# Performance work log

Measured on AMD Instinct MI355X. Metric: run time of the kernel, lower is better.

Reference implementation:

```python
import jax, jax.numpy as jnp
import numpy as np

N, E, D, H, C = 40000, 640000, 128, 4, 32  # nodes, edges, in_hid, heads, out_channels/head
NUM_NODE_TYPE, NUM_EDGE_TYPE = 8, 8
NEG_SLOPE = 0.2
EDGE_TYPE_SELF = 0


def setup_inputs() -> dict:
    key = jax.random.key(0)
    ks = jax.random.split(key, 12)
    x = jax.random.normal(ks[0], (N, D), dtype=jnp.float32)
    # build edges with no self-loops (the module filters src==dst before adding self-loops)
    src = jax.random.randint(ks[1], (E,), 0, N, dtype=jnp.int32)
    off = jax.random.randint(ks[2], (E,), 1, N, dtype=jnp.int32)
    dst = (src + off) % N
    edge_index = jnp.stack([src, dst])  # [2, E]
    node_type = jax.random.randint(ks[3], (N,), 0, NUM_NODE_TYPE, dtype=jnp.int32)
    edge_type = jax.random.randint(ks[4], (E,), 0, NUM_EDGE_TYPE, dtype=jnp.int32)
    g = 0.05
    Wq = jax.random.normal(ks[5], (H * C, D), dtype=jnp.float32) * g
    Wk = jax.random.normal(ks[6], (H * C, D), dtype=jnp.float32) * g
    Wv = jax.random.normal(ks[7], (H * C, D), dtype=jnp.float32) * g
    att_i = jax.random.normal(ks[8], (1, H, C), dtype=jnp.float32) * g
    att_j = jax.random.normal(ks[9], (1, H, C), dtype=jnp.float32) * g
    bias = jnp.zeros((H * C,), dtype=jnp.float32)
    node_emb_table = jax.random.normal(ks[10], (NUM_NODE_TYPE, D), dtype=jnp.float32) * g
    edge_emb_table = jax.random.normal(ks[11], (NUM_EDGE_TYPE, D), dtype=jnp.float32) * g
    return {"x": x, "edge_index": edge_index, "node_type": node_type,
            "edge_type": edge_type, "Wq": Wq, "Wk": Wk, "Wv": Wv,
            "att_i": att_i, "att_j": att_j, "bias": bias,
            "node_emb_table": node_emb_table, "edge_emb_table": edge_emb_table}


def reference(x, edge_index, node_type, edge_type, Wq, Wk, Wv,
              att_i, att_j, bias, node_emb_table, edge_emb_table):
    n = x.shape[0]
    # node-type embedding add
    x = x + node_emb_table[node_type]                       # [N, D]
    xq = x @ Wq.T                                           # [N, H*C]
    # add self-loops (input edges contain no src==dst by construction)
    self_idx = jnp.arange(n, dtype=edge_index.dtype)
    src = jnp.concatenate([edge_index[0], self_idx])        # [E+N]
    dst = jnp.concatenate([edge_index[1], self_idx])        # [E+N]
    et = jnp.concatenate([edge_type,
                          jnp.full((n,), EDGE_TYPE_SELF, dtype=edge_type.dtype)])
    edge_emb = edge_emb_table[et]                           # [E+N, D]
    # message: per-edge gather + K/V linear + additive attention
    x_j = x[src] + edge_emb                                 # [E+N, D]
    xq_i = xq[dst].reshape(-1, H, C)                        # [E+N, H, C]
    x_k = (x_j @ Wk.T).reshape(-1, H, C)
    x_v = (x_j @ Wv.T).reshape(-1, H, C)
    alpha = (xq_i * att_i).sum(-1) + (x_k * att_j).sum(-1)  # [E+N, H]
    alpha = jax.nn.leaky_relu(alpha, NEG_SLOPE)
    # segment softmax over destination nodes (PyG softmax, eps=1e-16)
    amax = jax.ops.segment_max(alpha, dst, num_segments=n)  # [N, H]
    alpha = jnp.exp(alpha - amax[dst])
    denom = jax.ops.segment_sum(alpha, dst, num_segments=n)
    alpha = alpha / (denom[dst] + 1e-16)
    # scatter-add weighted values
    out = jax.ops.segment_sum(x_v * alpha[..., None], dst, num_segments=n)  # [N, H, C]
    return out.reshape(n, H * C) + bias
```

## Files before the change

### kernel.cpp

```cpp
#include <hip/hip_runtime.h>
#include <math.h>

#define NN 40000
#define NE 640000
#define D 128
#define NH 4
#define NC 32
#define NEG 0.2f

#define NBKT 1250
#define NBIN 250
#define SEGC 16

typedef __attribute__((ext_vector_type(8))) short bf16x8;
typedef __attribute__((ext_vector_type(4))) float f32x4;

__device__ __forceinline__ unsigned pack_bf16(float a, float b) {
  unsigned ua = __float_as_uint(a), ub = __float_as_uint(b);
  ua = (ua + 0x7FFFu + ((ua >> 16) & 1u)) >> 16;
  ub = (ub + 0x7FFFu + ((ub >> 16) & 1u)) & 0xFFFF0000u;
  return ub | ua;
}

__device__ __forceinline__ bf16x8 to_bf16x8(float4 a, float4 b) {
  union { bf16x8 v; unsigned u[4]; } r;
  r.u[0] = pack_bf16(a.x, a.y);
  r.u[1] = pack_bf16(a.z, a.w);
  r.u[2] = pack_bf16(b.x, b.y);
  r.u[3] = pack_bf16(b.z, b.w);
  return r.v;
}

__device__ __forceinline__ float4 f4add(float4 a, float4 b) {
  return make_float4(a.x + b.x, a.y + b.y, a.z + b.z, a.w + b.w);
}

__global__ __launch_bounds__(1024) void k_pb(
    const int* __restrict__ ei, const int* __restrict__ etype,
    unsigned* __restrict__ binbuf,
    const float* __restrict__ Wq, const float* __restrict__ Wk,
    const float* __restrict__ Wv,
    const float* __restrict__ att_i, const float* __restrict__ att_j,
    const float* __restrict__ eemb,
    float* __restrict__ ev, float* __restrict__ a_et,
    unsigned* __restrict__ Wvh) {
  __shared__ unsigned smem[10640];
  int b = blockIdx.x, t = threadIdx.x;

  if (b < NBIN) {
    unsigned* lbuf = smem;
    int* hist = (int*)(smem + 10000);
    int e0 = b * 2560;
#pragma unroll 1
    for (int pass = 0; pass < 2; ++pass) {
      int bk0 = pass * 625;
      for (int j = t; j < 625; j += 1024) hist[j] = 0;
      __syncthreads();
#pragma unroll
      for (int k = 0; k < 3; ++k) {
        int ee = k * 1024 + t;
        if (ee < 2560) {
          int e = e0 + ee;
          int src = ei[e];
          int dst = ei[NE + e];
          int et  = etype[e];
          int bk = (dst >> 5) - bk0;
          if (bk >= 0 && bk < 625) {
            int r = atomicAdd(&hist[bk], 1);
            if (r < SEGC)
              lbuf[bk * SEGC + r] =
                  (unsigned)src | ((unsigned)et << 16) | ((unsigned)(dst & 31) << 19);
          }
        }
      }
      __syncthreads();
      for (int j = t; j < 625; j += 1024) {
        unsigned c = (unsigned)min(hist[j], SEGC);
        unsigned s0 = (c == 0) ? 0u : (lbuf[j * SEGC] & 0x01FFFFFFu);
        lbuf[j * SEGC] = s0 | (c << 27);
      }
      __syncthreads();
      for (int j = t; j < 625; j += 1024) {
        const uint4* __restrict__ s4 = (const uint4*)(lbuf + j * SEGC);
        uint4* __restrict__ d4 =
            (uint4*)(binbuf + ((size_t)(bk0 + j) * NBIN + b) * SEGC);
        d4[0] = s4[0]; d4[1] = s4[1]; d4[2] = s4[2]; d4[3] = s4[3];
      }
      __syncthreads();
    }
    return;
  }

  float* sm = (float*)smem;
  int tb = b - NBIN;
  if (tb == 0) {
    for (int j = t; j < 1024; j += 1024) {
      int isq = (j < 512);
      int h = (j >> 7) & 3, d = j & 127;
      const float* __restrict__ Wm = isq ? Wq : Wk;
      const float* __restrict__ am = isq ? att_i : att_j;
      float s = 0.f;
#pragma unroll
      for (int c = 0; c < NC; ++c) s = fmaf(am[h * NC + c], Wm[(h * NC + c) * D + d], s);
      sm[j] = s;
    }
    __syncthreads();
    for (int j = t; j < 1024; j += 1024) {
      int r = j >> 6;
      int c2 = (j & 63) * 2;
      float a = 0.f, bb = 0.f;
      if (r < 8) { a = sm[r * 128 + c2]; bb = sm[r * 128 + c2 + 1]; }
      Wvh[(128 + r) * 64 + (j & 63)] = pack_bf16(a, bb);
    }
    if (t < 32) {
      int ty = t >> 2, hh = t & 3;
      const float* wrow = sm + 512 + hh * 128;
      const float* __restrict__ emb = eemb + ty * D;
      float s = 0.f;
#pragma unroll 8
      for (int d = 0; d < D; ++d) s = fmaf(wrow[d], emb[d], s);
      a_et[t] = s;
    }
  } else if (tb <= 8) {
    int ty = tb - 1;
    if (t < 128) sm[t] = eemb[ty * D + t];
    __syncthreads();
    if (t < 128) {
      const float4* __restrict__ wr = (const float4*)(Wv + (size_t)t * D);
      const float4* __restrict__ er = (const float4*)sm;
      float s = 0.f;
#pragma unroll
      for (int k = 0; k < 32; ++k) {
        float4 ww = wr[k], ee = er[k];
        s = fmaf(ww.x, ee.x, s); s = fmaf(ww.y, ee.y, s);
        s = fmaf(ww.z, ee.z, s); s = fmaf(ww.w, ee.w, s);
      }
      ev[ty * D + t] = s;
    }
  } else {
    int j0 = (tb - 9) * 1024;
    for (int j = j0 + t; j < j0 + 1024; j += 1024)
      Wvh[j] = pack_bf16(Wv[2 * j], Wv[2 * j + 1]);
  }
}

__global__ __launch_bounds__(64) void k_xv(
    const float* __restrict__ x, const int* __restrict__ node_type,
    const float* __restrict__ nemb, const unsigned* __restrict__ Wvh,
    unsigned* __restrict__ xvh, float* __restrict__ aq, float* __restrict__ ak) {
  int bb = blockIdx.x, l = threadIdx.x;
  int quad = l >> 4, col = l & 15;
  int n0w = bb * 16;
  int node = n0w + col;
  int ntA = node_type[node];
  const float4* __restrict__ xr = (const float4*)(x + (size_t)node * D);
  const float4* __restrict__ nr = (const float4*)(nemb + (size_t)ntA * D);
  bf16x8 afr[4];
#pragma unroll
  for (int s = 0; s < 4; ++s) {
    const float4* p = xr + s * 8 + quad * 2;
    const float4* q4 = nr + s * 8 + quad * 2;
    afr[s] = to_bf16x8(f4add(p[0], q4[0]), f4add(p[1], q4[1]));
  }
  f32x4 acc[9];
#pragma unroll
  for (int ct = 0; ct < 9; ++ct) acc[ct] = (f32x4){0.f, 0.f, 0.f, 0.f};
#pragma unroll
  for (int ct = 0; ct < 9; ++ct) {
    const unsigned* __restrict__ brow = Wvh + (size_t)(ct * 16 + col) * 64;
#pragma unroll
    for (int s = 0; s < 4; ++s) {
      bf16x8 bfr = *(const bf16x8*)(brow + s * 16 + quad * 4);
      acc[ct] = __builtin_amdgcn_mfma_f32_16x16x32_bf16(afr[s], bfr, acc[ct], 0, 0, 0);
    }
  }
  int nodes[4];
#pragma unroll
  for (int r = 0; r < 4; ++r) nodes[r] = n0w + quad * 4 + r;
#pragma unroll
  for (int ct = 0; ct < 8; ++ct) {
#pragma unroll
    for (int r = 0; r < 4; ++r) {
      float val = acc[ct][r];
      float pv = __shfl_xor(val, 1);
      if (!(col & 1)) {
        xvh[nodes[r] * 64 + ct * 8 + (col >> 1)] = pack_bf16(val, pv);
      }
    }
  }
  if (col < 4) {
#pragma unroll
    for (int r = 0; r < 4; ++r) aq[nodes[r] * NH + col] = acc[8][r];
  } else if (col < 8) {
#pragma unroll
    for (int r = 0; r < 4; ++r) ak[nodes[r] * NH + (col - 4)] = acc[8][r];
  }
}

__global__ __launch_bounds__(512) void k_gb(
    const unsigned* __restrict__ binbuf,
    const float* __restrict__ aq, const float* __restrict__ ak,
    const float* __restrict__ a_et, const unsigned* __restrict__ xvh,
    const float* __restrict__ ev, const float* __restrict__ bias,
    float* __restrict__ out) {
  __shared__ int lcnt[32];
  __shared__ unsigned csr[2048];
  int b = blockIdx.x, t = threadIdx.x;
  if (t < 32) lcnt[t] = 0;
  __syncthreads();
  if (t < 2 * NBIN) {
    int seg = t >> 1, half = t & 1;
    const unsigned* __restrict__ sp = binbuf + ((size_t)b * NBIN + seg) * SEGC;
    int cnt = (int)(sp[0] >> 27);
    int base = half * 8;
    if (cnt > base) {
      uint4 a0 = *(const uint4*)(sp + base);
      uint4 a1 = *(const uint4*)(sp + base + 4);
      unsigned rr[8] = {a0.x, a0.y, a0.z, a0.w, a1.x, a1.y, a1.z, a1.w};
      if (half == 0) rr[0] &= 0x01FFFFFFu;
      int jn = min(cnt - base, 8);
#pragma unroll
      for (int j = 0; j < 8; ++j) {
        if (j < jn) {
          unsigned rec = rr[j];
          int loc = (int)(rec >> 19) & 31;
          int r = atomicAdd(&lcnt[loc], 1);
          if (r < 63) csr[(loc << 6) + r] = rec & 0x7FFFFu;
        }
      }
    }
  }
  __syncthreads();
  int w = t >> 6, l = t & 63;
  int g = l >> 3, q = l & 7;
  int h = q >> 1;
  const uint4* __restrict__ xv4 = (const uint4*)xvh;
  const float4* __restrict__ ep = (const float4*)(ev + g * D + 16 * q);
  float4 ea0 = ep[0], ea1 = ep[1], ea2 = ep[2], ea3 = ep[3];
#pragma unroll 1
  for (int j4 = 0; j4 < 4; ++j4) {
    int loc = (w << 2) + j4;
    int n = (b << 5) + loc;
    float aqh = aq[n * NH + h];
    int deg = min(lcnt[loc], 63);
    int m = deg + 1;
    float acc[16];
#pragma unroll
    for (int k = 0; k < 16; ++k) acc[k] = 0.f;
    float ps[8];
#pragma unroll
    for (int k = 0; k < 8; ++k) ps[k] = 0.f;
    int iters = (m + 7) >> 3;
    int i = g;
    bool val = (i < m);
    unsigned rec = (val && i < deg) ? csr[(loc << 6) + i] : (unsigned)n;
    int src = (int)(rec & 0xFFFFu), etc = (int)(rec >> 16);
    float sA = ak[src * NH + h] + a_et[etc * NH + h];
    uint4 vb0 = xv4[src * 16 + 2 * q];
    uint4 vb1 = xv4[src * 16 + 2 * q + 1];
    for (int it = 0; it < iters; ++it) {
      int i2 = i + 8;
      bool v2 = (i2 < m);
      float sAn = 0.f; int etn = 0;
      uint4 vb0n = make_uint4(0, 0, 0, 0), vb1n = make_uint4(0, 0, 0, 0);
      if (it + 1 < iters) {
        unsigned rec2 = (v2 && i2 < deg) ? csr[(loc << 6) + i2] : (unsigned)n;
        int s2 = (int)(rec2 & 0xFFFFu);
        etn = (int)(rec2 >> 16);
        sAn = ak[s2 * NH + h] + a_et[etn * NH + h];
        vb0n = xv4[s2 * 16 + 2 * q];
        vb1n = xv4[s2 * 16 + 2 * q + 1];
      }
      float s = aqh + sA;
      s = (s > 0.f) ? s : NEG * s;
      float p = val ? __expf(s) : 0.f;
#pragma unroll
      for (int tt = 0; tt < 8; ++tt) ps[tt] += (etc == tt) ? p : 0.f;
      float f[16];
      f[0]  = __uint_as_float(vb0.x << 16); f[1]  = __uint_as_float(vb0.x & 0xFFFF0000u);
      f[2]  = __uint_as_float(vb0.y << 16); f[3]  = __uint_as_float(vb0.y & 0xFFFF0000u);
      f[4]  = __uint_as_float(vb0.z << 16); f[5]  = __uint_as_float(vb0.z & 0xFFFF0000u);
      f[6]  = __uint_as_float(vb0.w << 16); f[7]  = __uint_as_float(vb0.w & 0xFFFF0000u);
      f[8]  = __uint_as_float(vb1.x << 16); f[9]  = __uint_as_float(vb1.x & 0xFFFF0000u);
      f[10] = __uint_as_float(vb1.y << 16); f[11] = __uint_as_float(vb1.y & 0xFFFF0000u);
      f[12] = __uint_as_float(vb1.z << 16); f[13] = __uint_as_float(vb1.z & 0xFFFF0000u);
      f[14] = __uint_as_float(vb1.w << 16); f[15] = __uint_as_float(vb1.w & 0xFFFF0000u);
#pragma unroll
      for (int k = 0; k < 16; ++k) acc[k] = fmaf(p, f[k], acc[k]);
      i = i2; val = v2; sA = sAn; etc = etn; vb0 = vb0n; vb1 = vb1n;
    }
#pragma unroll
    for (int tt = 0; tt < 8; ++tt) {
      ps[tt] += __shfl_xor(ps[tt], 8);
      ps[tt] += __shfl_xor(ps[tt], 16);
      ps[tt] += __shfl_xor(ps[tt], 32);
    }
    float dsum = ((ps[0] + ps[1]) + (ps[2] + ps[3])) + ((ps[4] + ps[5]) + (ps[6] + ps[7]));
    float psg = ps[0];
#pragma unroll
    for (int tt = 1; tt < 8; ++tt) psg = (g == tt) ? ps[tt] : psg;
    acc[0]  = fmaf(psg, ea0.x, acc[0]);
    acc[1]  = fmaf(psg, ea0.y, acc[1]);
    acc[2]  = fmaf(psg, ea0.z, acc[2]);
    acc[3]  = fmaf(psg, ea0.w, acc[3]);
    acc[4]  = fmaf(psg, ea1.x, acc[4]);
    acc[5]  = fmaf(psg, ea1.y, acc[5]);
    acc[6]  = fmaf(psg, ea1.z, acc[6]);
    acc[7]  = fmaf(psg, ea1.w, acc[7]);
    acc[8]  = fmaf(psg, ea2.x, acc[8]);
    acc[9]  = fmaf(psg, ea2.y, acc[9]);
    acc[10] = fmaf(psg, ea2.z, acc[10]);
    acc[11] = fmaf(psg, ea2.w, acc[11]);
    acc[12] = fmaf(psg, ea3.x, acc[12]);
    acc[13] = fmaf(psg, ea3.y, acc[13]);
    acc[14] = fmaf(psg, ea3.z, acc[14]);
    acc[15] = fmaf(psg, ea3.w, acc[15]);
#pragma unroll
    for (int k = 0; k < 16; ++k) {
      acc[k] += __shfl_xor(acc[k], 8);
      acc[k] += __shfl_xor(acc[k], 16);
      acc[k] += __shfl_xor(acc[k], 32);
    }
    if (g == 0) {
      float inv = 1.f / (dsum + 1e-16f);
      const float4* __restrict__ b4 = (const float4*)(bias + 16 * q);
      float4* __restrict__ op = (float4*)(out + (size_t)n * D + 16 * q);
#pragma unroll
      for (int k4 = 0; k4 < 4; ++k4) {
        float4 bb = b4[k4];
        op[k4] = make_float4(acc[4 * k4 + 0] * inv + bb.x,
                             acc[4 * k4 + 1] * inv + bb.y,
                             acc[4 * k4 + 2] * inv + bb.z,
                             acc[4 * k4 + 3] * inv + bb.w);
      }
    }
  }
}

extern "C" void kernel_launch(void* const* d_in, const int* in_sizes, int n_in,
                              void* d_out, int out_size, void* d_ws, size_t ws_size,
                              hipStream_t stream) {
  const float* x      = (const float*)d_in[0];
  const int*   ei     = (const int*)d_in[1];
  const int*   ntype  = (const int*)d_in[2];
  const int*   etype  = (const int*)d_in[3];
  const float* Wq     = (const float*)d_in[4];
  const float* Wk     = (const float*)d_in[5];
  const float* Wv     = (const float*)d_in[6];
  const float* att_i  = (const float*)d_in[7];
  const float* att_j  = (const float*)d_in[8];
  const float* bias   = (const float*)d_in[9];
  const float* nemb   = (const float*)d_in[10];
  const float* eemb   = (const float*)d_in[11];
  float* out = (float*)d_out;

  float* ws     = (float*)d_ws;
  unsigned* xvh = (unsigned*)ws;
  float* aq     = ws + (size_t)NN * 64;
  float* ak     = aq + NN * NH;
  float* ev     = ak + NN * NH;
  float* a_et   = ev + 1024;
  unsigned* Wvh = (unsigned*)(a_et + 32);
  unsigned* binbuf = (unsigned*)(Wvh + 9216);

  k_pb<<<dim3(NBIN + 17), dim3(1024), 0, stream>>>(ei, etype, binbuf,
                                                   Wq, Wk, Wv, att_i, att_j, eemb,
                                                   ev, a_et, Wvh);
  k_xv<<<dim3(2500), dim3(64), 0, stream>>>(x, ntype, nemb, Wvh, xvh, aq, ak);
  k_gb<<<dim3(NBKT), dim3(512), 0, stream>>>(binbuf, aq, ak, a_et,
                                             xvh, ev, bias, out);
}
```

Baseline: 166.3 us.

## Replace fixed-capacity edge bins with compact per-block counting-sort and offset table

The edge binning kernel now runs a two-pass counting sort per block: a histogram of destination buckets, a shared-memory prefix scan, then a compact scatter of packed edge records into a contiguous per-block buffer, plus a global offset/count table. The gather kernel reads each block's offset and count and walks the records serially instead of reading fixed 16-slot segments. This removes the padded 16-entry-per-segment writes and reads, shrinking global traffic and dropping the silent capacity overflow. In exchange it adds a Hillis-Steele scan with many barriers and a serial variable-length loop per thread in the gather stage.

```diff
diff --git a/kernel.cpp b/kernel.cpp
--- a/kernel.cpp
+++ b/kernel.cpp
@@ -10,7 +10,6 @@
 
 #define NBKT 1250
 #define NBIN 250
-#define SEGC 16
 
 typedef __attribute__((ext_vector_type(8))) short bf16x8;
 typedef __attribute__((ext_vector_type(4))) float f32x4;
@@ -37,57 +36,67 @@
 
 __global__ __launch_bounds__(1024) void k_pb(
     const int* __restrict__ ei, const int* __restrict__ etype,
-    unsigned* __restrict__ binbuf,
+    unsigned* __restrict__ obuf, unsigned* __restrict__ binbuf,
     const float* __restrict__ Wq, const float* __restrict__ Wk,
     const float* __restrict__ Wv,
     const float* __restrict__ att_i, const float* __restrict__ att_j,
     const float* __restrict__ eemb,
     float* __restrict__ ev, float* __restrict__ a_et,
     unsigned* __restrict__ Wvh) {
-  __shared__ unsigned smem[10640];
+  __shared__ unsigned smem[6400];
   int b = blockIdx.x, t = threadIdx.x;
 
   if (b < NBIN) {
-    unsigned* lbuf = smem;
-    int* hist = (int*)(smem + 10000);
+    int* hist = (int*)smem;
+    unsigned* sA = smem + 1280;
+    unsigned* sB = smem + 2560;
+    unsigned* lbuf = smem + 3840;
     int e0 = b * 2560;
-#pragma unroll 1
-    for (int pass = 0; pass < 2; ++pass) {
-      int bk0 = pass * 625;
-      for (int j = t; j < 625; j += 1024) hist[j] = 0;
+    for (int j = t; j < NBKT; j += 1024) hist[j] = 0;
+    __syncthreads();
+#pragma unroll
+    for (int k = 0; k < 3; ++k) {
+      int ee = k * 1024 + t;
+      if (ee < 2560) atomicAdd(&hist[ei[NE + e0 + ee] >> 5], 1);
+    }
+    __syncthreads();
+    for (int j = t; j < NBKT; j += 1024) sA[j] = (unsigned)hist[j];
+    __syncthreads();
+    unsigned* pin = sA;
+    unsigned* pout = sB;
+    for (int d = 1; d < NBKT; d <<= 1) {
+      for (int j = t; j < NBKT; j += 1024)
+        pout[j] = pin[j] + ((j >= d) ? pin[j - d] : 0u);
       __syncthreads();
-#pragma unroll
-      for (int k = 0; k < 3; ++k) {
-        int ee = k * 1024 + t;
-        if (ee < 2560) {
-          int e = e0 + ee;
-          int src = ei[e];
-          int dst = ei[NE + e];
-          int et  = etype[e];
-          int bk = (dst >> 5) - bk0;
-          if (bk >= 0 && bk < 625) {
-            int r = atomicAdd(&hist[bk], 1);
-            if (r < SEGC)
-              lbuf[bk * SEGC + r] =
-                  (unsigned)src | ((unsigned)et << 16) | ((unsigned)(dst & 31) << 19);
-          }
-        }
-      }
-      __syncthreads();
-      for (int j = t; j < 625; j += 1024) {
-        unsigned c = (unsigned)min(hist[j], SEGC);
-        unsigned s0 = (c == 0) ? 0u : (lbuf[j * SEGC] & 0x01FFFFFFu);
-        lbuf[j * SEGC] = s0 | (c << 27);
-      }
-      __syncthreads();
-      for (int j = t; j < 625; j += 1024) {
-        const uint4* __restrict__ s4 = (const uint4*)(lbuf + j * SEGC);
-        uint4* __restrict__ d4 =
-            (uint4*)(binbuf + ((size_t)(bk0 + j) * NBIN + b) * SEGC);
-        d4[0] = s4[0]; d4[1] = s4[1]; d4[2] = s4[2]; d4[3] = s4[3];
-      }
-      __syncthreads();
-    }
+      unsigned* tmp = pin; pin = pout; pout = tmp;
+    }
+    for (int j = t; j < NBKT; j += 1024) {
+      unsigned cnt = (unsigned)hist[j];
+      unsigned off = pin[j] - cnt;
+      pout[j] = off;
+      obuf[b * NBKT + j] = off | (cnt << 16);
+    }
+    __syncthreads();
+    for (int j = t; j < NBKT; j += 1024) hist[j] = 0;
+    __syncthreads();
+#pragma unroll
+    for (int k = 0; k < 3; ++k) {
+      int ee = k * 1024 + t;
+      if (ee < 2560) {
+        int e = e0 + ee;
+        int src = ei[e];
+        int dst = ei[NE + e];
+        int et  = etype[e];
+        int bk = dst >> 5;
+        int r = atomicAdd(&hist[bk], 1);
+        lbuf[pout[bk] + r] =
+            (unsigned)src | ((unsigned)et << 16) | ((unsigned)(dst & 31) << 19);
+      }
+    }
+    __syncthreads();
+    const uint4* __restrict__ ls = (const uint4*)lbuf;
+    uint4* __restrict__ gb4 = (uint4*)(binbuf + (size_t)b * 2560);
+    for (int j = t; j < 640; j += 1024) gb4[j] = ls[j];
     return;
   }
 
@@ -198,7 +207,7 @@
 }
 
 __global__ __launch_bounds__(512) void k_gb(
-    const unsigned* __restrict__ binbuf,
+    const unsigned* __restrict__ obuf, const unsigned* __restrict__ binbuf,
     const float* __restrict__ aq, const float* __restrict__ ak,
     const float* __restrict__ a_et, const unsigned* __restrict__ xvh,
     const float* __restrict__ ev, const float* __restrict__ bias,
@@ -208,26 +217,16 @@
   int b = blockIdx.x, t = threadIdx.x;
   if (t < 32) lcnt[t] = 0;
   __syncthreads();
-  if (t < 2 * NBIN) {
-    int seg = t >> 1, half = t & 1;
-    const unsigned* __restrict__ sp = binbuf + ((size_t)b * NBIN + seg) * SEGC;
-    int cnt = (int)(sp[0] >> 27);
-    int base = half * 8;
-    if (cnt > base) {
-      uint4 a0 = *(const uint4*)(sp + base);
-      uint4 a1 = *(const uint4*)(sp + base + 4);
-      unsigned rr[8] = {a0.x, a0.y, a0.z, a0.w, a1.x, a1.y, a1.z, a1.w};
-      if (half == 0) rr[0] &= 0x01FFFFFFu;
-      int jn = min(cnt - base, 8);
-#pragma unroll
-      for (int j = 0; j < 8; ++j) {
-        if (j < jn) {
-          unsigned rec = rr[j];
-          int loc = (int)(rec >> 19) & 31;
-          int r = atomicAdd(&lcnt[loc], 1);
-          if (r < 63) csr[(loc << 6) + r] = rec & 0x7FFFFu;
-        }
-      }
+  if (t < NBIN) {
+    unsigned oc = obuf[t * NBKT + b];
+    int off = (int)(oc & 0xFFFFu);
+    int cnt = (int)(oc >> 16);
+    const unsigned* __restrict__ rp = binbuf + (size_t)t * 2560 + off;
+    for (int j = 0; j < cnt; ++j) {
+      unsigned rec = rp[j];
+      int loc = (int)(rec >> 19) & 31;
+      int r = atomicAdd(&lcnt[loc], 1);
+      if (r < 63) csr[(loc << 6) + r] = rec & 0x7FFFFu;
     }
   }
   __syncthreads();
@@ -361,12 +360,13 @@
   float* ev     = ak + NN * NH;
   float* a_et   = ev + 1024;
   unsigned* Wvh = (unsigned*)(a_et + 32);
-  unsigned* binbuf = (unsigned*)(Wvh + 9216);
-
-  k_pb<<<dim3(NBIN + 17), dim3(1024), 0, stream>>>(ei, etype, binbuf,
+  unsigned* obuf = (unsigned*)(Wvh + 9216);
+  unsigned* binbuf = obuf + 312512;
+
+  k_pb<<<dim3(NBIN + 17), dim3(1024), 0, stream>>>(ei, etype, obuf, binbuf,
                                                    Wq, Wk, Wv, att_i, att_j, eemb,
                                                    ev, a_et, Wvh);
   k_xv<<<dim3(2500), dim3(64), 0, stream>>>(x, ntype, nemb, Wvh, xvh, aq, ak);
-  k_gb<<<dim3(NBKT), dim3(512), 0, stream>>>(binbuf, aq, ak, a_et,
+  k_gb<<<dim3(NBKT), dim3(512), 0, stream>>>(obuf, binbuf, aq, ak, a_et,
                                              xvh, ev, bias, out);
 }
```

New measurement: 168.5 us. About the same (+1.3%).
